# Kernel tuning notes

Hardware: AMD Instinct MI355X
Metric: run time of the kernel (lower is better)

## Reference

```python
import jax, jax.numpy as jnp
import numpy as np

HIDDEN = 4096
NUM_HEADS = 32
HEAD_DIM = 128
NUM_KV_HEADS = 8
KV_GROUPS = NUM_HEADS // NUM_KV_HEADS
ROPE_THETA = 10000.0
SEQ = 2048
BATCH = 1
NEG_INF = -1e9


def fake_quant_int8(x):
    """Per-tensor symmetric int8 fake quantization (absmax scale)."""
    scale = jnp.maximum(jnp.max(jnp.abs(x)) / 127.0, 1e-8)
    q = jnp.clip(jnp.round(x / scale), -127.0, 127.0) * scale
    # straight-through estimator (no-op in fwd-only, keeps code shared)
    return x + jax.lax.stop_gradient(q - x)


def rotate_half(x):
    x1, x2 = jnp.split(x, 2, axis=-1)
    return jnp.concatenate([-x2, x1], axis=-1)


def rope_cos_sin(position_ids):
    inv_freq = 1.0 / (ROPE_THETA ** (jnp.arange(0, HEAD_DIM, 2, dtype=jnp.float32) / HEAD_DIM))
    freqs = position_ids.astype(jnp.float32)[..., None] * inv_freq  # [B,S,HD/2]
    emb = jnp.concatenate([freqs, freqs], axis=-1)                  # [B,S,HD]
    return jnp.cos(emb), jnp.sin(emb)


def setup_inputs() -> dict:
    key = jax.random.key(0)
    k1, k2, k3, k4, k5 = jax.random.split(key, 5)
    hidden_states = jax.random.normal(k1, (BATCH, SEQ, HIDDEN), dtype=jnp.float32)
    causal = jnp.tril(jnp.ones((SEQ, SEQ), dtype=bool))
    attention_mask = jnp.where(causal, 0.0, NEG_INF).astype(jnp.float32)[None, None]  # [1,1,S,S]
    position_ids = jnp.arange(SEQ, dtype=jnp.int64 if jax.config.jax_enable_x64 else jnp.int32)[None, :]
    s = 0.02
    wq = jax.random.normal(k2, (NUM_HEADS * HEAD_DIM, HIDDEN), dtype=jnp.float32) * s
    wk = jax.random.normal(k3, (NUM_KV_HEADS * HEAD_DIM, HIDDEN), dtype=jnp.float32) * s
    wv = jax.random.normal(k4, (NUM_KV_HEADS * HEAD_DIM, HIDDEN), dtype=jnp.float32) * s
    wo = jax.random.normal(k5, (HIDDEN, NUM_HEADS * HEAD_DIM), dtype=jnp.float32) * s
    return {"hidden_states": hidden_states, "attention_mask": attention_mask,
            "position_ids": position_ids, "wq": wq, "wk": wk, "wv": wv, "wo": wo}


def reference(hidden_states, attention_mask, position_ids, wq, wk, wv, wo):
    B, S, _ = hidden_states.shape

    def qlinear(x, w):  # quantized linear: fake-quant act and weight, y = x @ w.T
        return fake_quant_int8(x) @ fake_quant_int8(w).T

    q = qlinear(hidden_states, wq).reshape(B, S, NUM_HEADS, HEAD_DIM).transpose(0, 2, 1, 3)
    k = qlinear(hidden_states, wk).reshape(B, S, NUM_KV_HEADS, HEAD_DIM).transpose(0, 2, 1, 3)
    v = qlinear(hidden_states, wv).reshape(B, S, NUM_KV_HEADS, HEAD_DIM).transpose(0, 2, 1, 3)

    cos, sin = rope_cos_sin(position_ids)      # [B,S,HD]
    cos, sin = cos[:, None], sin[:, None]      # [B,1,S,HD]
    q = q * cos + rotate_half(q) * sin
    k = k * cos + rotate_half(k) * sin

    # repeat_kv: GQA -> full heads
    k = jnp.repeat(k, KV_GROUPS, axis=1)
    v = jnp.repeat(v, KV_GROUPS, axis=1)

    # quantized QK^T
    scores = jnp.einsum('bhqd,bhkd->bhqk', fake_quant_int8(q), fake_quant_int8(k))
    scores = scores * (1.0 / np.sqrt(HEAD_DIM).astype(np.float32))
    scores = scores + attention_mask[:, :, :, :S]
    probs = jax.nn.softmax(scores.astype(jnp.float32), axis=-1).astype(q.dtype)
    # attention_dropout = 0.0 -> identity

    # quantized AV
    attn_out = jnp.einsum('bhqk,bhkd->bhqd', fake_quant_int8(probs), fake_quant_int8(v))
    attn_out = attn_out.transpose(0, 2, 1, 3).reshape(B, S, NUM_HEADS * HEAD_DIM)
    return qlinear(attn_out, wo)
```

## Files before the change

kernel.cpp:

```cpp
#include <hip/hip_runtime.h>
#include <hip/hip_fp16.h>
#include <stdint.h>

#define SEQ   2048
#define HID   4096
#define NH    32
#define NKV   8
#define KVDIM 1024
#define KVCAT 2048

typedef int v4i __attribute__((ext_vector_type(4)));

#define VMCNT0 asm volatile("s_waitcnt vmcnt(0)" ::: "memory")

__device__ __forceinline__ void gload16(const void* g, void* l) {
    __builtin_amdgcn_global_load_lds(
        (const __attribute__((address_space(1))) void*)(uintptr_t)g,
        (__attribute__((address_space(3))) void*)(uintptr_t)l, 16, 0, 0);
}

__device__ __forceinline__ float slot_scale(const unsigned* slots, int slot) {
    return fmaxf(__uint_as_float(slots[slot << 5]) / 127.0f, 1e-8f);
}

__device__ __forceinline__ int q8v(float x, float s) {
    int v = (int)rintf(x / s);
    return v < -127 ? -127 : (v > 127 ? 127 : v);
}

__device__ __forceinline__ unsigned pk4(float a, float b, float c, float d, float s) {
    return (unsigned)(uint8_t)(int8_t)q8v(a, s)
         | ((unsigned)(uint8_t)(int8_t)q8v(b, s) << 8)
         | ((unsigned)(uint8_t)(int8_t)q8v(c, s) << 16)
         | ((unsigned)(uint8_t)(int8_t)q8v(d, s) << 24);
}

__device__ __forceinline__ float fexp2(float x) {
    float r; asm("v_exp_f32 %0, %1" : "=v"(r) : "v"(x)); return r;
}

__device__ __forceinline__ float fmax4a(float4 x) {
    return fmaxf(fmaxf(fabsf(x.x), fabsf(x.y)), fmaxf(fabsf(x.z), fabsf(x.w)));
}

__device__ __forceinline__ void block_amax_part(float m, float* dst) {
    __shared__ float sm[4];
    int lane = threadIdx.x & 63, w = threadIdx.x >> 6;
    for (int off = 32; off; off >>= 1) m = fmaxf(m, __shfl_xor(m, off, 64));
    if (lane == 0) sm[w] = m;
    __syncthreads();
    if (threadIdx.x == 0)
        *dst = fmaxf(fmaxf(sm[0], sm[1]), fmaxf(sm[2], sm[3]));
    __syncthreads();
}

#define NV0 ((long)SEQ * HID / 4)
#define NV1 ((long)HID * HID / 4)
#define NV2 ((long)KVDIM * HID / 4)
__global__ void k_absmax5(const float* __restrict__ a0, const float* __restrict__ a1,
                          const float* __restrict__ a2, const float* __restrict__ a3,
                          const float* __restrict__ a4, float* __restrict__ part) {
    int b = blockIdx.x;
    const float* p; long n; int lb, nb;
    if (b < 342)       { p = a0; n = NV0; lb = b;        nb = 342; }
    else if (b < 1025) { p = a1; n = NV1; lb = b - 342;  nb = 683; }
    else if (b < 1196) { p = a2; n = NV2; lb = b - 1025; nb = 171; }
    else if (b < 1367) { p = a3; n = NV2; lb = b - 1196; nb = 171; }
    else               { p = a4; n = NV1; lb = b - 1367; nb = 681; }
    long str = (long)nb * 256;
    float mm[8] = {0.f, 0.f, 0.f, 0.f, 0.f, 0.f, 0.f, 0.f};
    long v = (long)lb * 256 + threadIdx.x;
    for (; v + 7 * str < n; v += 8 * str) {
        float4 t[8];
        #pragma unroll
        for (int j = 0; j < 8; j++) t[j] = *(const float4*)(p + (v + j * str) * 4);
        #pragma unroll
        for (int j = 0; j < 8; j++) mm[j] = fmaxf(mm[j], fmax4a(t[j]));
    }
    for (; v < n; v += str) mm[0] = fmaxf(mm[0], fmax4a(*(const float4*)(p + v * 4)));
    float m = fmaxf(fmaxf(fmaxf(mm[0], mm[1]), fmaxf(mm[2], mm[3])),
                    fmaxf(fmaxf(mm[4], mm[5]), fmaxf(mm[6], mm[7])));
    block_amax_part(m, part + blockIdx.x);
}

__global__ void k_reduceA(const float* __restrict__ part, unsigned* slots) {
    __shared__ float sm[4];
    const int lo[5] = {0, 342, 1025, 1196, 1367};
    const int hi[5] = {342, 1025, 1196, 1367, 2048};
    int t = threadIdx.x, lane = t & 63, w = t >> 6;
    for (int s = 0; s < 5; s++) {
        float m = 0.f;
        for (int i = lo[s] + t; i < hi[s]; i += 256) m = fmaxf(m, part[i]);
        for (int off = 32; off; off >>= 1) m = fmaxf(m, __shfl_xor(m, off, 64));
        if (lane == 0) sm[w] = m;
        __syncthreads();
        if (t == 0)
            slots[s << 5] = __float_as_uint(fmaxf(fmaxf(sm[0], sm[1]), fmaxf(sm[2], sm[3])));
        __syncthreads();
    }
}

__global__ void k_reduceB(const float* __restrict__ p1, const float* __restrict__ p2,
                          const float* __restrict__ p3, unsigned* slots) {
    __shared__ float sm[4];
    int t = threadIdx.x, lane = t & 63, w = t >> 6;
    const float* ps[3] = {p1, p2, p3};
    const int cnt[3] = {512, 128, 128};
    const int sl[3] = {5, 6, 7};
    for (int s = 0; s < 3; s++) {
        float m = 0.f;
        for (int i = t; i < cnt[s]; i += 256) m = fmaxf(m, ps[s][i]);
        for (int off = 32; off; off >>= 1) m = fmaxf(m, __shfl_xor(m, off, 64));
        if (lane == 0) sm[w] = m;
        __syncthreads();
        if (t == 0)
            slots[sl[s] << 5] = __float_as_uint(fmaxf(fmaxf(sm[0], sm[1]), fmaxf(sm[2], sm[3])));
        __syncthreads();
    }
}

#define NU0 ((long)SEQ * HID / 16)
#define NU1 ((long)HID * HID / 16)
#define NU2 ((long)KVDIM * HID / 16)
__global__ void k_quant4(const float* __restrict__ a0, const float* __restrict__ a1,
                         const float* __restrict__ a2, const float* __restrict__ a3,
                         int8_t* __restrict__ d0, int8_t* __restrict__ d1,
                         int8_t* __restrict__ d2, int8_t* __restrict__ d3,
                         const unsigned* __restrict__ slots) {
    int b = blockIdx.x;
    const float* p; int8_t* d; long n; int slot, lb, nb;
    if (b < 512)       { p = a0; d = d0; n = NU0; slot = 0; lb = b;        nb = 512; }
    else if (b < 1536) { p = a1; d = d1; n = NU1; slot = 1; lb = b - 512;  nb = 1024; }
    else if (b < 1792) { p = a2; d = d2; n = NU2; slot = 2; lb = b - 1536; nb = 256; }
    else               { p = a3; d = d3; n = NU2; slot = 3; lb = b - 1792; nb = 256; }
    float s = slot_scale(slots, slot);
    long str = (long)nb * 256;
    for (long u = (long)lb * 256 + threadIdx.x; u < n; u += str) {
        const float4* src = (const float4*)(p + u * 16);
        float4 t0 = src[0], t1 = src[1], t2 = src[2], t3 = src[3];
        int4 o;
        o.x = (int)pk4(t0.x, t0.y, t0.z, t0.w, s);
        o.y = (int)pk4(t1.x, t1.y, t1.z, t1.w, s);
        o.z = (int)pk4(t2.x, t2.y, t2.z, t2.w, s);
        o.w = (int)pk4(t3.x, t3.y, t3.z, t3.w, s);
        *(int4*)(d + u * 16) = o;
    }
}

__global__ void k_quantw(const float* __restrict__ x, int8_t* __restrict__ q, long nu,
                         const unsigned* __restrict__ slots, int slot) {
    float s = slot_scale(slots, slot);
    long gs = (long)gridDim.x * blockDim.x;
    for (long u = blockIdx.x * (long)blockDim.x + threadIdx.x; u < nu; u += gs) {
        const float4* src = (const float4*)(x + u * 16);
        float4 t0 = src[0], t1 = src[1], t2 = src[2], t3 = src[3];
        int4 o;
        o.x = (int)pk4(t0.x, t0.y, t0.z, t0.w, s);
        o.y = (int)pk4(t1.x, t1.y, t1.z, t1.w, s);
        o.z = (int)pk4(t2.x, t2.y, t2.z, t2.w, s);
        o.w = (int)pk4(t3.x, t3.y, t3.z, t3.w, s);
        *(int4*)(q + u * 16) = o;
    }
}

__device__ __forceinline__ unsigned pk4h(unsigned h2a, unsigned h2b, float s) {
    __half2 a = *(__half2*)&h2a, b = *(__half2*)&h2b;
    return pk4(__low2float(a), __high2float(a), __low2float(b), __high2float(b), s);
}
__global__ void k_quanth(const __half* __restrict__ x, int8_t* __restrict__ q, long nu,
                         int rshift, long cmask, long ld,
                         const unsigned* __restrict__ slots, int slot) {
    float s = slot_scale(slots, slot);
    long gs = (long)gridDim.x * blockDim.x;
    for (long u = blockIdx.x * (long)blockDim.x + threadIdx.x; u < nu; u += gs) {
        long row = u >> rshift;
        long cu = u & cmask;
        const int4* src = (const int4*)(x + row * ld + cu * 16);
        int4 a = src[0], b = src[1];
        int4 o;
        o.x = (int)pk4h((unsigned)a.x, (unsigned)a.y, s);
        o.y = (int)pk4h((unsigned)a.z, (unsigned)a.w, s);
        o.z = (int)pk4h((unsigned)b.x, (unsigned)b.y, s);
        o.w = (int)pk4h((unsigned)b.z, (unsigned)b.w, s);
        *(int4*)(q + u * 16) = o;
    }
}

__global__ void k_ropetab(const int* __restrict__ pos, float* __restrict__ ct,
                          float* __restrict__ st) {
    int tid = blockIdx.x * blockDim.x + threadIdx.x;
    if (tid >= SEQ * 64) return;
    int i = tid & 63, s = tid >> 6;
    double inv = 1.0 / pow(10000.0, (double)((float)(2 * i) * (1.0f / 128.0f)));
    float invf = (float)inv;
    float angf = (float)pos[s] * invf;
    double a = (double)angf;
    ct[tid] = (float)cos(a);
    st[tid] = (float)sin(a);
}

__global__ void k_transq(const __half* __restrict__ src, long lds_, int8_t* __restrict__ dst,
                         long ldd, const unsigned* __restrict__ slots, int slot) {
    __shared__ float t[32][33];
    float s = slot_scale(slots, slot);
    int bx = blockIdx.x, by = blockIdx.y;
    int tid = threadIdx.x;
    int c = tid & 31, r0 = tid >> 5;
    #pragma unroll
    for (int j = 0; j < 4; j++) {
        int r = r0 + j * 8;
        t[r][c] = __half2float(src[(long)(by * 32 + r) * lds_ + bx * 32 + c]);
    }
    __syncthreads();
    int d = tid >> 3, k4 = (tid & 7) * 4;
    unsigned pa = 0;
    #pragma unroll
    for (int j = 0; j < 4; j++) {
        int iv = q8v(t[k4 + j][d], s);
        pa |= ((unsigned)(uint8_t)(int8_t)iv) << (8 * j);
    }
    *(unsigned*)(dst + (long)(bx * 32 + d) * ldd + by * 32 + k4) = pa;
}

__global__ __launch_bounds__(256) void k_gemm_i8(
    const int8_t* __restrict__ A, const int8_t* __restrict__ B, void* __restrict__ Cv,
    int M, int N, int K, unsigned* slots,
    int slotA, int slotB, int slotB2, int nsplit,
    float* pQ, float* pK, float* pV, int ropemode,
    const float* __restrict__ ct, const float* __restrict__ st) {
    __shared__ int8_t POOL[65536];
    int8_t (*As)[16384] = (int8_t(*)[16384])POOL;
    int8_t (*Bs)[16384] = (int8_t(*)[16384])(POOL + 32768);
    float* Cf = (float*)Cv;
    __half* Ch = (__half*)Cv;
    const v4i vzero = {0, 0, 0, 0};
    int tid = threadIdx.x, lane = tid & 63, wid = tid >> 6;
    int nbx = N >> 7;
    int nwg = gridDim.x, wg = blockIdx.x;
    int cpx = nwg >> 3;
    int swz = (wg & 7) * cpx + (wg >> 3);
    int bm = swz / nbx, bn = swz % nbx;
    long rowA0 = (long)bm * 128, colB0 = (long)bn * 128;
    int wrow = (wid >> 1) * 64, wcol = (wid & 1) * 64;
    int lr = lane >> 3;
    int swc = ((lane & 7) ^ lr) * 16;
    const int8_t* ga = A + (rowA0 + wid * 8 + lr) * (long)K + swc;
    const int8_t* gb = B + (colB0 + wid * 8 + lr) * (long)K + swc;
    v4i acc[4][4];
    #pragma unroll
    for (int m = 0; m < 4; m++)
        #pragma unroll
        for (int n = 0; n < 4; n++) acc[m][n] = vzero;

    auto STAGE = [&](int buf, int kt) {
        #pragma unroll
        for (int i = 0; i < 4; i++) {
            gload16(ga + kt + (long)(i * 32) * K, &As[buf][(wid * 8 + i * 32) * 128]);
            gload16(gb + kt + (long)(i * 32) * K, &Bs[buf][(wid * 8 + i * 32) * 128]);
        }
    };
    auto COMPUTE = [&](int buf) {
        #pragma unroll
        for (int ks = 0; ks < 2; ks++) {
            v4i af[4], bf[4];
            #pragma unroll
            for (int m = 0; m < 4; m++) {
                int row = wrow + m * 16 + (lane & 15);
                af[m] = *(const v4i*)(&As[buf][row * 128 + (((ks * 4 + (lane >> 4)) ^ (row & 7)) * 16)]);
            }
            #pragma unroll
            for (int n = 0; n < 4; n++) {
                int row = wcol + n * 16 + (lane & 15);
                bf[n] = *(const v4i*)(&Bs[buf][row * 128 + (((ks * 4 + (lane >> 4)) ^ (row & 7)) * 16)]);
            }
            #pragma unroll
            for (int m = 0; m < 4; m++)
                #pragma unroll
                for (int n = 0; n < 4; n++)
                    acc[m][n] = __builtin_amdgcn_mfma_i32_16x16x64_i8(af[m], bf[n], acc[m][n], 0, 0, 0);
        }
    };

    STAGE(0, 0);
    VMCNT0;
    __syncthreads();
    int nt = K >> 7, cur = 0;
    for (int t = 0; t < nt - 1; t++) {
        STAGE(cur ^ 1, (t + 1) << 7);
        COMPUTE(cur);
        VMCNT0;
        __syncthreads();
        cur ^= 1;
    }
    COMPUTE(cur);

    float sA = slot_scale(slots, slotA);
    float sB1 = slot_scale(slots, slotB);
    float sB2 = slot_scale(slots, slotB2);
    int qc = lane & 15, rgrp = (lane >> 4) << 2;
    if (ropemode == 1 || (ropemode == 2 && bn < 8)) {
        __syncthreads();
        float* EX = (float*)POOL;
        #pragma unroll
        for (int m = 0; m < 4; m++)
            #pragma unroll
            for (int n = 0; n < 4; n++) {
                int coll = wcol + n * 16 + qc;
                #pragma unroll
                for (int r = 0; r < 4; r++) {
                    int rowl = wrow + m * 16 + rgrp + r;
                    EX[rowl * 128 + (coll ^ ((rowl & 1) << 4))] = sA * sB1 * (float)acc[m][n][r];
                }
            }
        __syncthreads();
        float am = 0.f;
        #pragma unroll
        for (int m = 0; m < 4; m++)
            #pragma unroll
            for (int n = 0; n < 4; n++) {
                int coll = wcol + n * 16 + qc;
                #pragma unroll
                for (int r = 0; r < 4; r++) {
                    int rowl = wrow + m * 16 + rgrp + r;
                    long srow = rowA0 + rowl;
                    float self = EX[rowl * 128 + (coll ^ ((rowl & 1) << 4))];
                    float pv = EX[rowl * 128 + ((coll ^ 64) ^ ((rowl & 1) << 4))];
                    float c = ct[srow * 64 + (coll & 63)];
                    float sn = st[srow * 64 + (coll & 63)];
                    float o = (coll < 64) ? self * c - pv * sn : self * c + pv * sn;
                    am = fmaxf(am, fabsf(o));
                    Ch[srow * N + colB0 + coll] = __float2half(o);
                }
            }
        block_amax_part(am, (ropemode == 1) ? pQ + blockIdx.x : pK + bm * 8 + (bn & 7));
    } else if (ropemode == 2) {
        float am = 0.f;
        #pragma unroll
        for (int m = 0; m < 4; m++) {
            long row0 = rowA0 + wrow + m * 16 + rgrp;
            #pragma unroll
            for (int n = 0; n < 4; n++) {
                int col = (int)colB0 + wcol + n * 16 + qc;
                float sc = sA * ((col < nsplit) ? sB1 : sB2);
                __half* cp = Ch + row0 * N + col;
                #pragma unroll
                for (int r = 0; r < 4; r++) {
                    float val = sc * (float)acc[m][n][r];
                    cp[(long)r * N] = __float2half(val);
                    am = fmaxf(am, fabsf(val));
                }
            }
        }
        block_amax_part(am, pV + bm * 8 + (bn & 7));
    } else {
        #pragma unroll
        for (int m = 0; m < 4; m++) {
            long row0 = rowA0 + wrow + m * 16 + rgrp;
            #pragma unroll
            for (int n = 0; n < 4; n++) {
                int col = (int)colB0 + wcol + n * 16 + qc;
                float sc = sA * ((col < nsplit) ? sB1 : sB2);
                float* cp = Cf + row0 * N + col;
                #pragma unroll
                for (int r = 0; r < 4; r++) cp[(long)r * N] = sc * (float)acc[m][n][r];
            }
        }
    }
}

__global__ __launch_bounds__(256) void k_attn(
    const int8_t* __restrict__ Qq, const int8_t* __restrict__ Kq, const int8_t* __restrict__ Vtq,
    __half* __restrict__ AO, unsigned* slots) {
    __shared__ int8_t Qs[64 * 128];
    __shared__ int8_t Ks[2][64 * 128];
    __shared__ int8_t Vs[2][128 * 64];
    __shared__ int smx[4];
    const v4i vzero = {0, 0, 0, 0};
    const int NEGS = -(1 << 29);
    const float MAGIC = 12582912.0f;
    int tid = threadIdx.x, lane = tid & 63, w = tid >> 6;
    int qlan = lane & 15, g = lane >> 4;
    int idx = blockIdx.x;
    int qb = 31 - (idx >> 5), h = idx & 31, kvh = h >> 2;
    float sq = slot_scale(slots, 5), sk = slot_scale(slots, 6);
    float spv = slot_scale(slots, 7) * (1.0f / 127.0f);
    float c2 = sq * sk * 0.08838834764831845f * 1.4426950408889634f;
    int lr8 = lane >> 3;
    int swc = ((lane & 7) ^ lr8) * 16;
    int lr4 = lane >> 2;
    int vswc = ((lane & 3) ^ (lr4 & 3)) * 16;
    const int8_t* kbase = Kq + ((long)(w * 8 + lr8)) * KVDIM + kvh * 128 + swc;
    const int8_t* vbase = Vtq + ((long)kvh * 128 + w * 16 + lr4) * SEQ + vswc;
    auto STAGE_K = [&](int buf, int kt) {
        #pragma unroll
        for (int i = 0; i < 2; i++)
            gload16(kbase + ((long)kt * 64 + i * 32) * KVDIM, &Ks[buf][(w * 8 + i * 32) * 128]);
    };
    auto STAGE_V = [&](int buf, int kt) {
        #pragma unroll
        for (int i = 0; i < 2; i++)
            gload16(vbase + (long)(i * 64) * SEQ + kt * 64, &Vs[buf][(w * 16 + i * 64) * 64]);
    };
    {
        const int8_t* qbase = Qq + ((long)qb * 64 + w * 8 + lr8) * HID + h * 128 + swc;
        #pragma unroll
        for (int i = 0; i < 2; i++)
            gload16(qbase + (long)(i * 32) * HID, &Qs[(w * 8 + i * 32) * 128]);
    }
    STAGE_K(0, 0);
    VMCNT0;
    __syncthreads();
    v4i aq[2];
    #pragma unroll
    for (int ks = 0; ks < 2; ks++) {
        int row = w * 16 + qlan;
        aq[ks] = *(const v4i*)(&Qs[row * 128 + (((ks * 4 + g) ^ (row & 7)) * 16)]);
    }
    int mi = -(1 << 30);
    float l = 0.f;
    int buf = 0;
    for (int kt = 0; kt <= qb; kt++) {
        if (kt < qb) STAGE_K(buf ^ 1, kt + 1);
        v4i sf[4] = {vzero, vzero, vzero, vzero};
        __builtin_amdgcn_s_setprio(1);
        #pragma unroll
        for (int ks = 0; ks < 2; ks++)
            #pragma unroll
            for (int f = 0; f < 4; f++) {
                int row = f * 16 + qlan;
                v4i bk = *(const v4i*)(&Ks[buf][row * 128 + (((ks * 4 + g) ^ (row & 7)) * 16)]);
                sf[f] = __builtin_amdgcn_mfma_i32_16x16x64_i8(bk, aq[ks], sf[f], 0, 0, 0);
            }
        __builtin_amdgcn_s_setprio(0);
        int sv[16];
        if (kt == qb) {
            int qthr = w * 16 + qlan;
            #pragma unroll
            for (int f = 0; f < 4; f++)
                #pragma unroll
                for (int r = 0; r < 4; r++) {
                    int kl = f * 16 + g * 4 + r;
                    sv[f * 4 + r] = (kl > qthr) ? NEGS : sf[f][r];
                }
        } else {
            #pragma unroll
            for (int f = 0; f < 4; f++)
                #pragma unroll
                for (int r = 0; r < 4; r++) sv[f * 4 + r] = sf[f][r];
        }
        int tm = sv[0];
        #pragma unroll
        for (int e = 1; e < 16; e++) tm = tm > sv[e] ? tm : sv[e];
        tm = max(tm, __shfl_xor(tm, 16, 64));
        tm = max(tm, __shfl_xor(tm, 32, 64));
        int mn = tm > mi ? tm : mi;
        float nb = -c2 * (float)mn;
        float esc = fexp2(fmaf((float)mi, c2, nb));
        float es = 0.f;
        #pragma unroll
        for (int e = 0; e < 16; e++) es += fexp2(fmaf((float)sv[e], c2, nb));
        es += __shfl_xor(es, 16, 64);
        es += __shfl_xor(es, 32, 64);
        l = l * esc + es;
        mi = mn;
        VMCNT0;
        __syncthreads();
        buf ^= 1;
    }
    float Bq = fmaf(c2, (float)mi, __log2f(l) - 6.9886846867721655f);
    unsigned* Ps32 = (unsigned*)Qs;
    int pwr = w * 320;
    v4i of[8];
    #pragma unroll
    for (int nf = 0; nf < 8; nf++) of[nf] = vzero;
    STAGE_K(0, 0);
    STAGE_V(0, 0);
    VMCNT0;
    __syncthreads();
    buf = 0;
    for (int kt = 0; kt <= qb; kt++) {
        if (kt < qb) { STAGE_K(buf ^ 1, kt + 1); STAGE_V(buf ^ 1, kt + 1); }
        v4i sf[4] = {vzero, vzero, vzero, vzero};
        __builtin_amdgcn_s_setprio(1);
        #pragma unroll
        for (int ks = 0; ks < 2; ks++)
            #pragma unroll
            for (int f = 0; f < 4; f++) {
                int row = f * 16 + qlan;
                v4i bk = *(const v4i*)(&Ks[buf][row * 128 + (((ks * 4 + g) ^ (row & 7)) * 16)]);
                sf[f] = __builtin_amdgcn_mfma_i32_16x16x64_i8(bk, aq[ks], sf[f], 0, 0, 0);
            }
        __builtin_amdgcn_s_setprio(0);
        if (kt == qb) {
            int qthr = w * 16 + qlan;
            #pragma unroll
            for (int f = 0; f < 4; f++) {
                unsigned pk = 0;
                #pragma unroll
                for (int r = 0; r < 4; r++) {
                    int kl = f * 16 + g * 4 + r;
                    int s = (kl > qthr) ? NEGS : sf[f][r];
                    float t = fexp2(fmaf((float)s, c2, -Bq));
                    unsigned u = __float_as_uint(t + MAGIC) & 127u;
                    pk |= u << (8 * r);
                }
                Ps32[pwr + (4 * f + g) * 20 + qlan] = pk;
            }
        } else {
            #pragma unroll
            for (int f = 0; f < 4; f++) {
                unsigned pk = 0;
                #pragma unroll
                for (int r = 0; r < 4; r++) {
                    float t = fexp2(fmaf((float)sf[f][r], c2, -Bq));
                    unsigned u = __float_as_uint(t + MAGIC) & 127u;
                    pk |= u << (8 * r);
                }
                Ps32[pwr + (4 * f + g) * 20 + qlan] = pk;
            }
        }
        int rb = pwr + 80 * g + qlan;
        v4i ap;
        ap[0] = (int)Ps32[rb];
        ap[1] = (int)Ps32[rb + 20];
        ap[2] = (int)Ps32[rb + 40];
        ap[3] = (int)Ps32[rb + 60];
        __builtin_amdgcn_s_setprio(1);
        #pragma unroll
        for (int nf = 0; nf < 8; nf++) {
            int row = nf * 16 + qlan;
            v4i bv = *(const v4i*)(&Vs[buf][row * 64 + ((g ^ (row & 3)) * 16)]);
            of[nf] = __builtin_amdgcn_mfma_i32_16x16x64_i8(ap, bv, of[nf], 0, 0, 0);
        }
        __builtin_amdgcn_s_setprio(0);
        VMCNT0;
        __syncthreads();
        buf ^= 1;
    }
    int mymax = 0;
    #pragma unroll
    for (int nf = 0; nf < 8; nf++)
        #pragma unroll
        for (int r = 0; r < 4; r++) {
            int val = of[nf][r];
            int av = val < 0 ? -val : val;
            mymax = av > mymax ? av : mymax;
            int qg = qb * 64 + w * 16 + 4 * g + r;
            AO[(long)qg * HID + h * 128 + nf * 16 + qlan] = __float2half(spv * (float)val);
        }
    #pragma unroll
    for (int off = 1; off < 64; off <<= 1) {
        int o2 = __shfl_xor(mymax, off, 64);
        mymax = o2 > mymax ? o2 : mymax;
    }
    if (lane == 0) smx[w] = mymax;
    __syncthreads();
    if (tid == 0) {
        int mm = max(max(smx[0], smx[1]), max(smx[2], smx[3]));
        atomicMax(slots + (8 << 5), (unsigned)mm);
    }
}

__global__ void k_quant_ao(const __half* __restrict__ a, int8_t* __restrict__ q,
                           unsigned* slots) {
    float sv = slot_scale(slots, 7);
    float spv = (1.0f / 127.0f) * sv;
    float amax = spv * (float)(int)slots[8 << 5];
    float s = fmaxf(amax / 127.0f, 1e-8f);
    long nu = (long)SEQ * HID / 16;
    long gs = (long)gridDim.x * blockDim.x;
    for (long u = blockIdx.x * (long)blockDim.x + threadIdx.x; u < nu; u += gs) {
        const int4* src = (const int4*)(a + u * 16);
        int4 x = src[0], y = src[1];
        int4 o;
        o.x = (int)pk4h((unsigned)x.x, (unsigned)x.y, s);
        o.y = (int)pk4h((unsigned)x.z, (unsigned)x.w, s);
        o.z = (int)pk4h((unsigned)y.x, (unsigned)y.y, s);
        o.w = (int)pk4h((unsigned)y.z, (unsigned)y.w, s);
        *(int4*)(q + u * 16) = o;
    }
    if (blockIdx.x == 0 && threadIdx.x == 0) slots[9 << 5] = __float_as_uint(amax);
}

extern "C" void kernel_launch(void* const* d_in, const int* in_sizes, int n_in,
                              void* d_out, int out_size, void* d_ws, size_t ws_size,
                              hipStream_t stream) {
    (void)in_sizes; (void)n_in; (void)out_size;
    const float* hid = (const float*)d_in[0];
    const int* pos = (const int*)d_in[2];
    const float* wqp = (const float*)d_in[3];
    const float* wkp = (const float*)d_in[4];
    const float* wvp = (const float*)d_in[5];
    const float* wop = (const float*)d_in[6];
    float* out = (float*)d_out;
    char* ws = (char*)d_ws;

    size_t o = 0;
    auto alloc = [&](size_t sz) { size_t r = o; o += (sz + 255) & ~(size_t)255; return r; };
    unsigned* slots = (unsigned*)(ws + alloc(2048));
    float* P0 = (float*)(ws + alloc(2048 * 4));
    float* P1 = (float*)(ws + alloc(512 * 4));
    float* P2 = (float*)(ws + alloc(128 * 4));
    float* P3 = (float*)(ws + alloc(128 * 4));
    int8_t* Xq   = (int8_t*)(ws + alloc((size_t)SEQ * HID));
    int8_t* Wqq  = (int8_t*)(ws + alloc((size_t)HID * HID));
    int8_t* Wkvq = (int8_t*)(ws + alloc((size_t)KVCAT * HID));
    __half* Qf   = (__half*)(ws + alloc((size_t)SEQ * HID * 2));
    __half* KVf  = (__half*)(ws + alloc((size_t)SEQ * KVCAT * 2));
    int8_t* Qq   = (int8_t*)(ws + alloc((size_t)SEQ * HID));
    int8_t* Kq   = (int8_t*)(ws + alloc((size_t)SEQ * KVDIM));
    int8_t* Vtq  = (int8_t*)(ws + alloc((size_t)KVDIM * SEQ));
    float*  ctab = (float*)(ws + alloc((size_t)SEQ * 64 * 4));
    float*  stab = (float*)(ws + alloc((size_t)SEQ * 64 * 4));
    if (ws_size < o) return;
    int8_t* Woq = Wqq;
    __half* AOh = Qf;
    int8_t* AOq = Xq;

    hipMemsetAsync(slots, 0, 2048, stream);
    k_ropetab<<<SEQ * 64 / 256, 256, 0, stream>>>(pos, ctab, stab);
    k_absmax5<<<2048, 256, 0, stream>>>(hid, wqp, wkp, wvp, wop, P0);
    k_reduceA<<<1, 256, 0, stream>>>(P0, slots);
    k_quant4<<<2048, 256, 0, stream>>>(hid, wqp, wkp, wvp,
                                       Xq, Wqq, Wkvq, Wkvq + (size_t)KVDIM * HID, slots);
    k_gemm_i8<<<512, 256, 0, stream>>>(Xq, Wqq, Qf, SEQ, HID, HID, slots,
                                       0, 1, 1, 1 << 30, P1, nullptr, nullptr, 1, ctab, stab);
    k_gemm_i8<<<256, 256, 0, stream>>>(Xq, Wkvq, KVf, SEQ, KVCAT, HID, slots,
                                       0, 2, 3, KVDIM, nullptr, P2, P3, 2, ctab, stab);
    k_quantw<<<1024, 256, 0, stream>>>(wop, Woq, (long)HID * HID / 16, slots, 4);
    k_reduceB<<<1, 256, 0, stream>>>(P1, P2, P3, slots);
    const long CALL = 0x3FFFFFFFL;
    k_quanth<<<1024, 256, 0, stream>>>(Qf, Qq, (long)SEQ * HID / 16, 40, CALL, 0, slots, 5);
    k_quanth<<<512, 256, 0, stream>>>(KVf, Kq, (long)SEQ * KVDIM / 16, 6, 63, KVCAT, slots, 6);
    k_transq<<<dim3(32, 64), 256, 0, stream>>>(KVf + KVDIM, KVCAT, Vtq, SEQ, slots, 7);
    k_attn<<<1024, 256, 0, stream>>>(Qq, Kq, Vtq, AOh, slots);
    k_quant_ao<<<1024, 256, 0, stream>>>(AOh, AOq, slots);
    k_gemm_i8<<<512, 256, 0, stream>>>(AOq, Woq, out, SEQ, HID, HID, slots,
                                       9, 4, 4, 1 << 30, nullptr, nullptr, nullptr, 0,
                                       nullptr, nullptr);
}
```

Measured before the change: 285.8 us.

## Merge Q/KV GEMMs, fold Wo quant into quant5, skip negligible attention tiles

Wo quantization moves into the combined quant kernel, and Wo gets its own buffer instead of aliasing Wq. The separate Q and KV projection GEMM launches become a single 768-block kernel, which removes a launch and the tail between them. In attention, the per-tile row max from the first pass is saved and reused: the second pass skips the QK recompute and the PV MFMAs for any key tile where every lane's quantized probability would round to zero. This skip keeps the result exact under int8 rounding, but it adds branch divergence and extra shared memory.

Result: slower. 301.3 us (+5.4%).

```diff
diff --git a/kernel.cpp b/kernel.cpp
--- a/kernel.cpp
+++ b/kernel.cpp
@@ -122,17 +122,20 @@
 #define NU0 ((long)SEQ * HID / 16)
 #define NU1 ((long)HID * HID / 16)
 #define NU2 ((long)KVDIM * HID / 16)
-__global__ void k_quant4(const float* __restrict__ a0, const float* __restrict__ a1,
+__global__ void k_quant5(const float* __restrict__ a0, const float* __restrict__ a1,
                          const float* __restrict__ a2, const float* __restrict__ a3,
+                         const float* __restrict__ a4,
                          int8_t* __restrict__ d0, int8_t* __restrict__ d1,
                          int8_t* __restrict__ d2, int8_t* __restrict__ d3,
+                         int8_t* __restrict__ d4,
                          const unsigned* __restrict__ slots) {
     int b = blockIdx.x;
     const float* p; int8_t* d; long n; int slot, lb, nb;
     if (b < 512)       { p = a0; d = d0; n = NU0; slot = 0; lb = b;        nb = 512; }
     else if (b < 1536) { p = a1; d = d1; n = NU1; slot = 1; lb = b - 512;  nb = 1024; }
     else if (b < 1792) { p = a2; d = d2; n = NU2; slot = 2; lb = b - 1536; nb = 256; }
-    else               { p = a3; d = d3; n = NU2; slot = 3; lb = b - 1792; nb = 256; }
+    else if (b < 2048) { p = a3; d = d3; n = NU2; slot = 3; lb = b - 1792; nb = 256; }
+    else               { p = a4; d = d4; n = NU1; slot = 4; lb = b - 2048; nb = 512; }
     float s = slot_scale(slots, slot);
     long str = (long)nb * 256;
     for (long u = (long)lb * 256 + threadIdx.x; u < n; u += str) {
@@ -144,22 +147,6 @@
         o.z = (int)pk4(t2.x, t2.y, t2.z, t2.w, s);
         o.w = (int)pk4(t3.x, t3.y, t3.z, t3.w, s);
         *(int4*)(d + u * 16) = o;
-    }
-}
-
-__global__ void k_quantw(const float* __restrict__ x, int8_t* __restrict__ q, long nu,
-                         const unsigned* __restrict__ slots, int slot) {
-    float s = slot_scale(slots, slot);
-    long gs = (long)gridDim.x * blockDim.x;
-    for (long u = blockIdx.x * (long)blockDim.x + threadIdx.x; u < nu; u += gs) {
-        const float4* src = (const float4*)(x + u * 16);
-        float4 t0 = src[0], t1 = src[1], t2 = src[2], t3 = src[3];
-        int4 o;
-        o.x = (int)pk4(t0.x, t0.y, t0.z, t0.w, s);
-        o.y = (int)pk4(t1.x, t1.y, t1.z, t1.w, s);
-        o.z = (int)pk4(t2.x, t2.y, t2.z, t2.w, s);
-        o.w = (int)pk4(t3.x, t3.y, t3.z, t3.w, s);
-        *(int4*)(q + u * 16) = o;
     }
 }
 
@@ -222,17 +209,142 @@
     *(unsigned*)(dst + (long)(bx * 32 + d) * ldd + by * 32 + k4) = pa;
 }
 
-__global__ __launch_bounds__(256) void k_gemm_i8(
-    const int8_t* __restrict__ A, const int8_t* __restrict__ B, void* __restrict__ Cv,
-    int M, int N, int K, unsigned* slots,
-    int slotA, int slotB, int slotB2, int nsplit,
-    float* pQ, float* pK, float* pV, int ropemode,
+__global__ __launch_bounds__(256) void k_gemm12(
+    const int8_t* __restrict__ Xq, const int8_t* __restrict__ Wqq,
+    const int8_t* __restrict__ Wkvq, __half* __restrict__ Qf, __half* __restrict__ KVf,
+    unsigned* slots, float* pQ, float* pK, float* pV,
     const float* __restrict__ ct, const float* __restrict__ st) {
     __shared__ int8_t POOL[65536];
     int8_t (*As)[16384] = (int8_t(*)[16384])POOL;
     int8_t (*Bs)[16384] = (int8_t(*)[16384])(POOL + 32768);
-    float* Cf = (float*)Cv;
-    __half* Ch = (__half*)Cv;
+    const v4i vzero = {0, 0, 0, 0};
+    int tid = threadIdx.x, lane = tid & 63, wid = tid >> 6;
+    int wg = blockIdx.x;
+    int swz = (wg & 7) * 96 + (wg >> 3);
+    int mode, bm, bn, N;
+    const int8_t* Bptr;
+    __half* Ch;
+    if (swz < 512) { mode = 1; bm = swz >> 5; bn = swz & 31; N = HID;   Bptr = Wqq;  Ch = Qf; }
+    else { int s2 = swz - 512; mode = 2; bm = s2 >> 4; bn = s2 & 15; N = KVCAT; Bptr = Wkvq; Ch = KVf; }
+    long rowA0 = (long)bm * 128, colB0 = (long)bn * 128;
+    int wrow = (wid >> 1) * 64, wcol = (wid & 1) * 64;
+    int lr = lane >> 3;
+    int swc = ((lane & 7) ^ lr) * 16;
+    const int8_t* ga = Xq + (rowA0 + wid * 8 + lr) * (long)HID + swc;
+    const int8_t* gb = Bptr + (colB0 + wid * 8 + lr) * (long)HID + swc;
+    v4i acc[4][4];
+    #pragma unroll
+    for (int m = 0; m < 4; m++)
+        #pragma unroll
+        for (int n = 0; n < 4; n++) acc[m][n] = vzero;
+
+    auto STAGE = [&](int buf, int kt) {
+        #pragma unroll
+        for (int i = 0; i < 4; i++) {
+            gload16(ga + kt + (long)(i * 32) * HID, &As[buf][(wid * 8 + i * 32) * 128]);
+            gload16(gb + kt + (long)(i * 32) * HID, &Bs[buf][(wid * 8 + i * 32) * 128]);
+        }
+    };
+    auto COMPUTE = [&](int buf) {
+        #pragma unroll
+        for (int ks = 0; ks < 2; ks++) {
+            v4i af[4], bf[4];
+            #pragma unroll
+            for (int m = 0; m < 4; m++) {
+                int row = wrow + m * 16 + (lane & 15);
+                af[m] = *(const v4i*)(&As[buf][row * 128 + (((ks * 4 + (lane >> 4)) ^ (row & 7)) * 16)]);
+            }
+            #pragma unroll
+            for (int n = 0; n < 4; n++) {
+                int row = wcol + n * 16 + (lane & 15);
+                bf[n] = *(const v4i*)(&Bs[buf][row * 128 + (((ks * 4 + (lane >> 4)) ^ (row & 7)) * 16)]);
+            }
+            #pragma unroll
+            for (int m = 0; m < 4; m++)
+                #pragma unroll
+                for (int n = 0; n < 4; n++)
+                    acc[m][n] = __builtin_amdgcn_mfma_i32_16x16x64_i8(af[m], bf[n], acc[m][n], 0, 0, 0);
+        }
+    };
+
+    STAGE(0, 0);
+    VMCNT0;
+    __syncthreads();
+    int cur = 0;
+    for (int t = 0; t < 31; t++) {
+        STAGE(cur ^ 1, (t + 1) << 7);
+        COMPUTE(cur);
+        VMCNT0;
+        __syncthreads();
+        cur ^= 1;
+    }
+    COMPUTE(cur);
+
+    float sA = slot_scale(slots, 0);
+    int qc = lane & 15, rgrp = (lane >> 4) << 2;
+    if (mode == 1 || bn < 8) {
+        float sB = slot_scale(slots, mode == 1 ? 1 : 2);
+        __syncthreads();
+        float* EX = (float*)POOL;
+        #pragma unroll
+        for (int m = 0; m < 4; m++)
+            #pragma unroll
+            for (int n = 0; n < 4; n++) {
+                int coll = wcol + n * 16 + qc;
+                #pragma unroll
+                for (int r = 0; r < 4; r++) {
+                    int rowl = wrow + m * 16 + rgrp + r;
+                    EX[rowl * 128 + (coll ^ ((rowl & 1) << 4))] = sA * sB * (float)acc[m][n][r];
+                }
+            }
+        __syncthreads();
+        float am = 0.f;
+        #pragma unroll
+        for (int m = 0; m < 4; m++)
+            #pragma unroll
+            for (int n = 0; n < 4; n++) {
+                int coll = wcol + n * 16 + qc;
+                #pragma unroll
+                for (int r = 0; r < 4; r++) {
+                    int rowl = wrow + m * 16 + rgrp + r;
+                    long srow = rowA0 + rowl;
+                    float self = EX[rowl * 128 + (coll ^ ((rowl & 1) << 4))];
+                    float pv = EX[rowl * 128 + ((coll ^ 64) ^ ((rowl & 1) << 4))];
+                    float c = ct[srow * 64 + (coll & 63)];
+                    float sn = st[srow * 64 + (coll & 63)];
+                    float o = (coll < 64) ? self * c - pv * sn : self * c + pv * sn;
+                    am = fmaxf(am, fabsf(o));
+                    Ch[srow * N + colB0 + coll] = __float2half(o);
+                }
+            }
+        block_amax_part(am, (mode == 1) ? pQ + swz : pK + bm * 8 + bn);
+    } else {
+        float sB = slot_scale(slots, 3);
+        float am = 0.f;
+        #pragma unroll
+        for (int m = 0; m < 4; m++) {
+            long row0 = rowA0 + wrow + m * 16 + rgrp;
+            #pragma unroll
+            for (int n = 0; n < 4; n++) {
+                int col = (int)colB0 + wcol + n * 16 + qc;
+                __half* cp = Ch + row0 * N + col;
+                #pragma unroll
+                for (int r = 0; r < 4; r++) {
+                    float val = sA * sB * (float)acc[m][n][r];
+                    cp[(long)r * N] = __float2half(val);
+                    am = fmaxf(am, fabsf(val));
+                }
+            }
+        }
+        block_amax_part(am, pV + bm * 8 + (bn - 8));
+    }
+}
+
+__global__ __launch_bounds__(256) void k_gemm_i8(
+    const int8_t* __restrict__ A, const int8_t* __restrict__ B, float* __restrict__ C,
+    int N, int K, unsigned* slots, int slotA, int slotB) {
+    __shared__ int8_t As[2][16384];
+    __shared__ int8_t Bs[2][16384];
     const v4i vzero = {0, 0, 0, 0};
     int tid = threadIdx.x, lane = tid & 63, wid = tid >> 6;
     int nbx = N >> 7;
@@ -294,76 +406,17 @@
     }
     COMPUTE(cur);
 
-    float sA = slot_scale(slots, slotA);
-    float sB1 = slot_scale(slots, slotB);
-    float sB2 = slot_scale(slots, slotB2);
+    float sc = slot_scale(slots, slotA) * slot_scale(slots, slotB);
     int qc = lane & 15, rgrp = (lane >> 4) << 2;
-    if (ropemode == 1 || (ropemode == 2 && bn < 8)) {
-        __syncthreads();
-        float* EX = (float*)POOL;
-        #pragma unroll
-        for (int m = 0; m < 4; m++)
-            #pragma unroll
-            for (int n = 0; n < 4; n++) {
-                int coll = wcol + n * 16 + qc;
-                #pragma unroll
-                for (int r = 0; r < 4; r++) {
-                    int rowl = wrow + m * 16 + rgrp + r;
-                    EX[rowl * 128 + (coll ^ ((rowl & 1) << 4))] = sA * sB1 * (float)acc[m][n][r];
-                }
-            }
-        __syncthreads();
-        float am = 0.f;
-        #pragma unroll
-        for (int m = 0; m < 4; m++)
-            #pragma unroll
-            for (int n = 0; n < 4; n++) {
-                int coll = wcol + n * 16 + qc;
-                #pragma unroll
-                for (int r = 0; r < 4; r++) {
-                    int rowl = wrow + m * 16 + rgrp + r;
-                    long srow = rowA0 + rowl;
-                    float self = EX[rowl * 128 + (coll ^ ((rowl & 1) << 4))];
-                    float pv = EX[rowl * 128 + ((coll ^ 64) ^ ((rowl & 1) << 4))];
-                    float c = ct[srow * 64 + (coll & 63)];
-                    float sn = st[srow * 64 + (coll & 63)];
-                    float o = (coll < 64) ? self * c - pv * sn : self * c + pv * sn;
-                    am = fmaxf(am, fabsf(o));
-                    Ch[srow * N + colB0 + coll] = __float2half(o);
-                }
-            }
-        block_amax_part(am, (ropemode == 1) ? pQ + blockIdx.x : pK + bm * 8 + (bn & 7));
-    } else if (ropemode == 2) {
-        float am = 0.f;
-        #pragma unroll
-        for (int m = 0; m < 4; m++) {
-            long row0 = rowA0 + wrow + m * 16 + rgrp;
-            #pragma unroll
-            for (int n = 0; n < 4; n++) {
-                int col = (int)colB0 + wcol + n * 16 + qc;
-                float sc = sA * ((col < nsplit) ? sB1 : sB2);
-                __half* cp = Ch + row0 * N + col;
-                #pragma unroll
-                for (int r = 0; r < 4; r++) {
-                    float val = sc * (float)acc[m][n][r];
-                    cp[(long)r * N] = __float2half(val);
-                    am = fmaxf(am, fabsf(val));
-                }
-            }
-        }
-        block_amax_part(am, pV + bm * 8 + (bn & 7));
-    } else {
-        #pragma unroll
-        for (int m = 0; m < 4; m++) {
-            long row0 = rowA0 + wrow + m * 16 + rgrp;
-            #pragma unroll
-            for (int n = 0; n < 4; n++) {
-                int col = (int)colB0 + wcol + n * 16 + qc;
-                float sc = sA * ((col < nsplit) ? sB1 : sB2);
-                float* cp = Cf + row0 * N + col;
-                #pragma unroll
-                for (int r = 0; r < 4; r++) cp[(long)r * N] = sc * (float)acc[m][n][r];
-            }
+    #pragma unroll
+    for (int m = 0; m < 4; m++) {
+        long row0 = rowA0 + wrow + m * 16 + rgrp;
+        #pragma unroll
+        for (int n = 0; n < 4; n++) {
+            int col = (int)colB0 + wcol + n * 16 + qc;
+            float* cp = C + row0 * N + col;
+            #pragma unroll
+            for (int r = 0; r < 4; r++) cp[(long)r * N] = sc * (float)acc[m][n][r];
         }
     }
 }
@@ -375,6 +428,7 @@
     __shared__ int8_t Ks[2][64 * 128];
     __shared__ int8_t Vs[2][128 * 64];
     __shared__ int smx[4];
+    __shared__ int tmx[4][32][16];
     const v4i vzero = {0, 0, 0, 0};
     const int NEGS = -(1 << 29);
     const float MAGIC = 12582912.0f;
@@ -453,6 +507,7 @@
         for (int e = 1; e < 16; e++) tm = tm > sv[e] ? tm : sv[e];
         tm = max(tm, __shfl_xor(tm, 16, 64));
         tm = max(tm, __shfl_xor(tm, 32, 64));
+        tmx[w][kt][qlan] = tm;
         int mn = tm > mi ? tm : mi;
         float nb = -c2 * (float)mn;
         float esc = fexp2(fmaf((float)mi, c2, nb));
@@ -480,59 +535,63 @@
     buf = 0;
     for (int kt = 0; kt <= qb; kt++) {
         if (kt < qb) { STAGE_K(buf ^ 1, kt + 1); STAGE_V(buf ^ 1, kt + 1); }
-        v4i sf[4] = {vzero, vzero, vzero, vzero};
-        __builtin_amdgcn_s_setprio(1);
-        #pragma unroll
-        for (int ks = 0; ks < 2; ks++)
-            #pragma unroll
-            for (int f = 0; f < 4; f++) {
-                int row = f * 16 + qlan;
-                v4i bk = *(const v4i*)(&Ks[buf][row * 128 + (((ks * 4 + g) ^ (row & 7)) * 16)]);
-                sf[f] = __builtin_amdgcn_mfma_i32_16x16x64_i8(bk, aq[ks], sf[f], 0, 0, 0);
-            }
-        __builtin_amdgcn_s_setprio(0);
-        if (kt == qb) {
-            int qthr = w * 16 + qlan;
-            #pragma unroll
-            for (int f = 0; f < 4; f++) {
-                unsigned pk = 0;
-                #pragma unroll
-                for (int r = 0; r < 4; r++) {
-                    int kl = f * 16 + g * 4 + r;
-                    int s = (kl > qthr) ? NEGS : sf[f][r];
-                    float t = fexp2(fmaf((float)s, c2, -Bq));
-                    unsigned u = __float_as_uint(t + MAGIC) & 127u;
-                    pk |= u << (8 * r);
+        int tmv = tmx[w][kt][qlan];
+        int act = (fmaf(c2, (float)tmv, -Bq) > -1.0f);
+        if (__any(act)) {
+            v4i sf[4] = {vzero, vzero, vzero, vzero};
+            __builtin_amdgcn_s_setprio(1);
+            #pragma unroll
+            for (int ks = 0; ks < 2; ks++)
+                #pragma unroll
+                for (int f = 0; f < 4; f++) {
+                    int row = f * 16 + qlan;
+                    v4i bk = *(const v4i*)(&Ks[buf][row * 128 + (((ks * 4 + g) ^ (row & 7)) * 16)]);
+                    sf[f] = __builtin_amdgcn_mfma_i32_16x16x64_i8(bk, aq[ks], sf[f], 0, 0, 0);
                 }
-                Ps32[pwr + (4 * f + g) * 20 + qlan] = pk;
-            }
-        } else {
-            #pragma unroll
-            for (int f = 0; f < 4; f++) {
-                unsigned pk = 0;
-                #pragma unroll
-                for (int r = 0; r < 4; r++) {
-                    float t = fexp2(fmaf((float)sf[f][r], c2, -Bq));
-                    unsigned u = __float_as_uint(t + MAGIC) & 127u;
-                    pk |= u << (8 * r);
+            __builtin_amdgcn_s_setprio(0);
+            if (kt == qb) {
+                int qthr = w * 16 + qlan;
+                #pragma unroll
+                for (int f = 0; f < 4; f++) {
+                    unsigned pk = 0;
+                    #pragma unroll
+                    for (int r = 0; r < 4; r++) {
+                        int kl = f * 16 + g * 4 + r;
+                        int s = (kl > qthr) ? NEGS : sf[f][r];
+                        float t = fexp2(fmaf((float)s, c2, -Bq));
+                        unsigned u = __float_as_uint(t + MAGIC) & 127u;
+                        pk |= u << (8 * r);
+                    }
+                    Ps32[pwr + (4 * f + g) * 20 + qlan] = pk;
                 }
-                Ps32[pwr + (4 * f + g) * 20 + qlan] = pk;
-            }
-        }
-        int rb = pwr + 80 * g + qlan;
-        v4i ap;
-        ap[0] = (int)Ps32[rb];
-        ap[1] = (int)Ps32[rb + 20];
-        ap[2] = (int)Ps32[rb + 40];
-        ap[3] = (int)Ps32[rb + 60];
-        __builtin_amdgcn_s_setprio(1);
-        #pragma unroll
-        for (int nf = 0; nf < 8; nf++) {
-            int row = nf * 16 + qlan;
-            v4i bv = *(const v4i*)(&Vs[buf][row * 64 + ((g ^ (row & 3)) * 16)]);
-            of[nf] = __builtin_amdgcn_mfma_i32_16x16x64_i8(ap, bv, of[nf], 0, 0, 0);
-        }
-        __builtin_amdgcn_s_setprio(0);
+            } else {
+                #pragma unroll
+                for (int f = 0; f < 4; f++) {
+                    unsigned pk = 0;
+                    #pragma unroll
+                    for (int r = 0; r < 4; r++) {
+                        float t = fexp2(fmaf((float)sf[f][r], c2, -Bq));
+                        unsigned u = __float_as_uint(t + MAGIC) & 127u;
+                        pk |= u << (8 * r);
+                    }
+                    Ps32[pwr + (4 * f + g) * 20 + qlan] = pk;
+                }
+            }
+            int rb = pwr + 80 * g + qlan;
+            v4i ap;
+            ap[0] = (int)Ps32[rb];
+            ap[1] = (int)Ps32[rb + 20];
+            ap[2] = (int)Ps32[rb + 40];
+            ap[3] = (int)Ps32[rb + 60];
+            __builtin_amdgcn_s_setprio(1);
+            #pragma unroll
+            for (int nf = 0; nf < 8; nf++) {
+                int row = nf * 16 + qlan;
+                v4i bv = *(const v4i*)(&Vs[buf][row * 64 + ((g ^ (row & 3)) * 16)]);
+                of[nf] = __builtin_amdgcn_mfma_i32_16x16x64_i8(ap, bv, of[nf], 0, 0, 0);
+            }
+            __builtin_amdgcn_s_setprio(0);
+        }
         VMCNT0;
         __syncthreads();
         buf ^= 1;
@@ -604,6 +663,7 @@
     float* P3 = (float*)(ws + alloc(128 * 4));
     int8_t* Xq   = (int8_t*)(ws + alloc((size_t)SEQ * HID));
     int8_t* Wqq  = (int8_t*)(ws + alloc((size_t)HID * HID));
+    int8_t* Woq  = (int8_t*)(ws + alloc((size_t)HID * HID));
     int8_t* Wkvq = (int8_t*)(ws + alloc((size_t)KVCAT * HID));
     __half* Qf   = (__half*)(ws + alloc((size_t)SEQ * HID * 2));
     __half* KVf  = (__half*)(ws + alloc((size_t)SEQ * KVCAT * 2));
@@ -613,7 +673,6 @@
     float*  ctab = (float*)(ws + alloc((size_t)SEQ * 64 * 4));
     float*  stab = (float*)(ws + alloc((size_t)SEQ * 64 * 4));
     if (ws_size < o) return;
-    int8_t* Woq = Wqq;
     __half* AOh = Qf;
     int8_t* AOq = Xq;
 
@@ -621,13 +680,10 @@
     k_ropetab<<<SEQ * 64 / 256, 256, 0, stream>>>(pos, ctab, stab);
     k_absmax5<<<2048, 256, 0, stream>>>(hid, wqp, wkp, wvp, wop, P0);
     k_reduceA<<<1, 256, 0, stream>>>(P0, slots);
-    k_quant4<<<2048, 256, 0, stream>>>(hid, wqp, wkp, wvp,
-                                       Xq, Wqq, Wkvq, Wkvq + (size_t)KVDIM * HID, slots);
-    k_gemm_i8<<<512, 256, 0, stream>>>(Xq, Wqq, Qf, SEQ, HID, HID, slots,
-                                       0, 1, 1, 1 << 30, P1, nullptr, nullptr, 1, ctab, stab);
-    k_gemm_i8<<<256, 256, 0, stream>>>(Xq, Wkvq, KVf, SEQ, KVCAT, HID, slots,
-                                       0, 2, 3, KVDIM, nullptr, P2, P3, 2, ctab, stab);
-    k_quantw<<<1024, 256, 0, stream>>>(wop, Woq, (long)HID * HID / 16, slots, 4);
+    k_quant5<<<2560, 256, 0, stream>>>(hid, wqp, wkp, wvp, wop,
+                                       Xq, Wqq, Wkvq, Wkvq + (size_t)KVDIM * HID, Woq, slots);
+    k_gemm12<<<768, 256, 0, stream>>>(Xq, Wqq, Wkvq, Qf, KVf, slots,
+                                      P1, P2, P3, ctab, stab);
     k_reduceB<<<1, 256, 0, stream>>>(P1, P2, P3, slots);
     const long CALL = 0x3FFFFFFFL;
     k_quanth<<<1024, 256, 0, stream>>>(Qf, Qq, (long)SEQ * HID / 16, 40, CALL, 0, slots, 5);
@@ -635,7 +691,5 @@
     k_transq<<<dim3(32, 64), 256, 0, stream>>>(KVf + KVDIM, KVCAT, Vtq, SEQ, slots, 7);
     k_attn<<<1024, 256, 0, stream>>>(Qq, Kq, Vtq, AOh, slots);
     k_quant_ao<<<1024, 256, 0, stream>>>(AOh, AOq, slots);
-    k_gemm_i8<<<512, 256, 0, stream>>>(AOq, Woq, out, SEQ, HID, HID, slots,
-                                       9, 4, 4, 1 << 30, nullptr, nullptr, nullptr, 0,
-                                       nullptr, nullptr);
-}
+    k_gemm_i8<<<512, 256, 0, stream>>>(AOq, Woq, out, HID, HID, slots, 9, 4);
+}
```
